# Optimization experiments

Hardware: AMD Instinct MI355X
Metric: run time of the kernel (lower is better)

The kernel has to match this reference:

```python
import jax, jax.numpy as jnp
import numpy as np


def setup_inputs() -> dict:
    key = jax.random.key(0)
    k1, k2 = jax.random.split(key)
    B, D, L = 8192, 256, 4
    x = jax.random.normal(k1, (B, D), dtype=jnp.float32)
    # nn.Linear(d,1) weights (one row per layer) with kaiming-uniform-like scale
    W = jax.random.normal(k2, (L, D), dtype=jnp.float32) * (1.0 / np.sqrt(D))
    b_lin = jnp.zeros((L,), dtype=jnp.float32)   # linear biases (scalar per layer)
    bias = jnp.zeros((L, D), dtype=jnp.float32)  # per-layer bias params (init zeros)
    return {"x": x, "W": W, "b_lin": b_lin, "bias": bias}


def reference(x, W, b_lin, bias):
    # DCN cross: x_l = x_0 (x_l^T w_i) + b_lin_i + bias_i + x_l
    # Mathematically identical to the torch outer-product form:
    #   (x_0 @ x_l^T) @ w_i + b_lin_i == x_0 * (x_l . w_i) + b_lin_i
    num_layers = W.shape[0]
    x_0 = x
    x_l = x
    for i in range(num_layers):
        s = x_l @ W[i]                                  # [B]  (x_l . w_i)
        x_l = x_0 * s[:, None] + b_lin[i] + bias[i][None, :] + x_l
    return x_l
```

## Files before the change

### kernel.cpp

```cpp
#include <hip/hip_runtime.h>


__global__ __launch_bounds__(256) void cross_kernel(
    const float* __restrict__ x,
    const float* __restrict__ W,
    const float* __restrict__ b_lin,
    const float* __restrict__ bias,
    float* __restrict__ out,
    int B, int L)
{
    const int wave = threadIdx.x >> 6;
    const int lane = threadIdx.x & 63;
    const int row  = blockIdx.x * 4 + wave;
    if (row >= B) return;

    const float4* xrow = (const float4*)(x + (size_t)row * 256);
    float4 x0 = xrow[lane];
    float4 xl = x0;

    #pragma unroll
    for (int i = 0; i < 4; ++i) {
        if (i >= L) break;
        float4 w = ((const float4*)(W + i * 256))[lane];
        float p = xl.x * w.x + xl.y * w.y + xl.z * w.z + xl.w * w.w;
        #pragma unroll
        for (int off = 32; off > 0; off >>= 1)
            p += __shfl_xor(p, off, 64);
        const float s = p;

        float4 bi = ((const float4*)(bias + i * 256))[lane];
        const float bl = b_lin[i];

        xl.x = fmaf(x0.x, s, bl + bi.x + xl.x);
        xl.y = fmaf(x0.y, s, bl + bi.y + xl.y);
        xl.z = fmaf(x0.z, s, bl + bi.z + xl.z);
        xl.w = fmaf(x0.w, s, bl + bi.w + xl.w);
    }

    ((float4*)(out + (size_t)row * 256))[lane] = xl;
}

extern "C" void kernel_launch(void* const* d_in, const int* in_sizes, int n_in,
                              void* d_out, int out_size, void* d_ws, size_t ws_size,
                              hipStream_t stream) {
    const float* x     = (const float*)d_in[0];
    const float* W     = (const float*)d_in[1];
    const float* b_lin = (const float*)d_in[2];
    const float* bias  = (const float*)d_in[3];
    float* out = (float*)d_out;

    const int L = in_sizes[2];
    const int D = in_sizes[1] / L;
    const int B = in_sizes[0] / D;

    const int rows_per_block = 4;
    const int grid = (B + rows_per_block - 1) / rows_per_block;
    cross_kernel<<<grid, 256, 0, stream>>>(x, W, b_lin, bias, out, B, L);
}
```

Before: 66.66 us.

## Algebraically collapse cross layers into independent dot products reduced together

Rewrites the layer recurrence in closed form: x_l = x0*t + P, where t and P follow from dot products of x0 and the cumulative biases with each weight row. All seven dot products are computed up front and reduced together in one interleaved shuffle tree, removing the serial dependency of four back-to-back wave reductions. It hardcodes L=4 and changes the floating-point summation order.

```diff
diff --git a/kernel.cpp b/kernel.cpp
--- a/kernel.cpp
+++ b/kernel.cpp
@@ -7,37 +7,65 @@
     const float* __restrict__ b_lin,
     const float* __restrict__ bias,
     float* __restrict__ out,
-    int B, int L)
+    int B)
 {
     const int wave = threadIdx.x >> 6;
     const int lane = threadIdx.x & 63;
     const int row  = blockIdx.x * 4 + wave;
     if (row >= B) return;
 
-    const float4* xrow = (const float4*)(x + (size_t)row * 256);
-    float4 x0 = xrow[lane];
-    float4 xl = x0;
+    const float4 x0 = ((const float4*)(x + (size_t)row * 256))[lane];
+
+    float4 w0 = ((const float4*)(W + 0 * 256))[lane];
+    float4 w1 = ((const float4*)(W + 1 * 256))[lane];
+    float4 w2 = ((const float4*)(W + 2 * 256))[lane];
+    float4 w3 = ((const float4*)(W + 3 * 256))[lane];
+
+    const float bl0 = b_lin[0], bl1 = b_lin[1], bl2 = b_lin[2], bl3 = b_lin[3];
+    float4 c0 = ((const float4*)(bias + 0 * 256))[lane];
+    float4 c1 = ((const float4*)(bias + 1 * 256))[lane];
+    float4 c2 = ((const float4*)(bias + 2 * 256))[lane];
+    float4 c3 = ((const float4*)(bias + 3 * 256))[lane];
+    c0.x += bl0; c0.y += bl0; c0.z += bl0; c0.w += bl0;
+    c1.x += bl1; c1.y += bl1; c1.z += bl1; c1.w += bl1;
+    c2.x += bl2; c2.y += bl2; c2.z += bl2; c2.w += bl2;
+    c3.x += bl3; c3.y += bl3; c3.z += bl3; c3.w += bl3;
+
+    float4 P1 = c0;
+    float4 P2 = {P1.x + c1.x, P1.y + c1.y, P1.z + c1.z, P1.w + c1.w};
+    float4 P3 = {P2.x + c2.x, P2.y + c2.y, P2.z + c2.z, P2.w + c2.w};
+    float4 PL = {P3.x + c3.x, P3.y + c3.y, P3.z + c3.z, P3.w + c3.w};
+
+    float v[7];
+    v[0] = x0.x * w0.x + x0.y * w0.y + x0.z * w0.z + x0.w * w0.w;
+    v[1] = x0.x * w1.x + x0.y * w1.y + x0.z * w1.z + x0.w * w1.w;
+    v[2] = x0.x * w2.x + x0.y * w2.y + x0.z * w2.z + x0.w * w2.w;
+    v[3] = x0.x * w3.x + x0.y * w3.y + x0.z * w3.z + x0.w * w3.w;
+    v[4] = P1.x * w1.x + P1.y * w1.y + P1.z * w1.z + P1.w * w1.w;
+    v[5] = P2.x * w2.x + P2.y * w2.y + P2.z * w2.z + P2.w * w2.w;
+    v[6] = P3.x * w3.x + P3.y * w3.y + P3.z * w3.z + P3.w * w3.w;
 
     #pragma unroll
-    for (int i = 0; i < 4; ++i) {
-        if (i >= L) break;
-        float4 w = ((const float4*)(W + i * 256))[lane];
-        float p = xl.x * w.x + xl.y * w.y + xl.z * w.z + xl.w * w.w;
+    for (int off = 32; off > 0; off >>= 1) {
         #pragma unroll
-        for (int off = 32; off > 0; off >>= 1)
-            p += __shfl_xor(p, off, 64);
-        const float s = p;
-
-        float4 bi = ((const float4*)(bias + i * 256))[lane];
-        const float bl = b_lin[i];
-
-        xl.x = fmaf(x0.x, s, bl + bi.x + xl.x);
-        xl.y = fmaf(x0.y, s, bl + bi.y + xl.y);
-        xl.z = fmaf(x0.z, s, bl + bi.z + xl.z);
-        xl.w = fmaf(x0.w, s, bl + bi.w + xl.w);
+        for (int k = 0; k < 7; ++k)
+            v[k] += __shfl_xor(v[k], off, 64);
     }
 
-    ((float4*)(out + (size_t)row * 256))[lane] = xl;
+    const float d0 = v[0], d1 = v[1], d2 = v[2], d3 = v[3];
+    const float e1 = v[4], e2 = v[5], e3 = v[6];
+    float t = 1.0f;
+    float s0 = t * d0;            t += s0;
+    float s1 = fmaf(t, d1, e1);   t += s1;
+    float s2 = fmaf(t, d2, e2);   t += s2;
+    float s3 = fmaf(t, d3, e3);   t += s3;
+
+    float4 o;
+    o.x = fmaf(x0.x, t, PL.x);
+    o.y = fmaf(x0.y, t, PL.y);
+    o.z = fmaf(x0.z, t, PL.z);
+    o.w = fmaf(x0.w, t, PL.w);
+    ((float4*)(out + (size_t)row * 256))[lane] = o;
 }
 
 extern "C" void kernel_launch(void* const* d_in, const int* in_sizes, int n_in,
@@ -53,7 +81,6 @@
     const int D = in_sizes[1] / L;
     const int B = in_sizes[0] / D;
 
-    const int rows_per_block = 4;
-    const int grid = (B + rows_per_block - 1) / rows_per_block;
-    cross_kernel<<<grid, 256, 0, stream>>>(x, W, b_lin, bias, out, B, L);
+    const int grid = (B + 3) / 4;
+    cross_kernel<<<grid, 256, 0, stream>>>(x, W, b_lin, bias, out, B);
 }
```

Result: no change. 67.73 us (+1.6%).
